# Kernel optimization log

Measured on AMD Instinct MI355X. Metric: run time of the kernel, lower is better.

## Reference

```python
import jax, jax.numpy as jnp
import numpy as np

B, C, D = 1024, 100, 768


def setup_inputs() -> dict:
    key = jax.random.key(0)
    k1, k2, k3, k4 = jax.random.split(key, 4)
    raw_features = jax.random.normal(k1, (B, D), dtype=jnp.float32)
    class_means = jax.random.normal(k2, (C, D), dtype=jnp.float32)
    # stand-in for per-class pinv of shrunk+normalized covariance
    class_inv_covs = jax.random.normal(k3, (C, D, D), dtype=jnp.float32) * 0.02
    # diag_std is positive (clamped at 1e-6 in the original)
    class_diags = jax.random.uniform(k4, (C, D), dtype=jnp.float32, minval=0.5, maxval=1.5)
    return {
        "raw_features": raw_features,
        "class_means": class_means,
        "class_inv_covs": class_inv_covs,
        "class_diags": class_diags,
    }


def reference(raw_features, class_means, class_inv_covs, class_diags):
    # Batched over classes: diff[b,c,d] = raw[b,d]/diag[c,d] - mean[c,d]/diag[c,d]
    diff = (raw_features[:, None, :] - class_means[None, :, :]) / class_diags[None, :, :]  # [B,C,D]
    # temp[b,c,e] = sum_d diff[b,c,d] * inv[c,d,e]  (the per-class diff @ inv_c)
    temp = jnp.einsum('bcd,cde->bce', diff, class_inv_covs)
    dist_sq = jnp.sum(temp * diff, axis=-1)  # [B,C]
    return -dist_sq  # scores_stack
```

## Files before the change

kernel.cpp:

```cpp
#include <hip/hip_runtime.h>
#include <hip/hip_bf16.h>

#define B_SZ 1024
#define C_SZ 100
#define D_SZ 768

#define BM 128
#define BN 256
#define BK 32
#define NKT (D_SZ / BK)
#define NTHREADS 512
#define TPC 24

#define A_HALF (BM * BK)
#define X_HALF (BN * BK)

#define TBL_ELEMS ((size_t)C_SZ * D_SZ)
#define AP_ELEMS  ((size_t)C_SZ * D_SZ * D_SZ)
#define RB_ELEMS  ((size_t)B_SZ * D_SZ)

typedef float f32x4 __attribute__((ext_vector_type(4)));
typedef short short8 __attribute__((ext_vector_type(8)));

__device__ __forceinline__ ushort f2bf(float f) {
    union { __hip_bfloat16 b; ushort u; } cv; cv.b = __float2bfloat16(f); return cv.u;
}
__device__ __forceinline__ float bf2f(ushort u) {
    union { __hip_bfloat16 b; ushort us; } cv; cv.us = u; return __bfloat162float(cv.b);
}
__device__ __forceinline__ void gload_lds16(const void* g, void* l) {
    __builtin_amdgcn_global_load_lds((const __attribute__((address_space(1))) void*)g,
                                     (__attribute__((address_space(3))) void*)l, 16, 0, 0);
}

__global__ __launch_bounds__(256) void prep_small(const float* __restrict__ mean,
                                                  const float* __restrict__ diag,
                                                  const float* __restrict__ raw,
                                                  float* __restrict__ rd,
                                                  float* __restrict__ md,
                                                  ushort* __restrict__ rb) {
    const int bx = (int)blockIdx.x;
    if (bx < 75) {
        const int i = (bx * 256 + (int)threadIdx.x) * 4;
        if (i < (int)TBL_ELEMS) {
            const f32x4 dv = *(const f32x4*)(diag + i);
            const f32x4 mv = *(const f32x4*)(mean + i);
            f32x4 r, m;
            r.x = 1.0f / dv.x; r.y = 1.0f / dv.y; r.z = 1.0f / dv.z; r.w = 1.0f / dv.w;
            m.x = mv.x * r.x;  m.y = mv.y * r.y;  m.z = mv.z * r.z;  m.w = mv.w * r.w;
            *(f32x4*)(rd + i) = r;
            *(f32x4*)(md + i) = m;
        }
    } else {
        const size_t i = (size_t)(bx - 75) * 256 + threadIdx.x;
        const f32x4 v0 = *(const f32x4*)(raw + i * 8);
        const f32x4 v1 = *(const f32x4*)(raw + i * 8 + 4);
        short8 p;
        p[0]=(short)f2bf(v0.x); p[1]=(short)f2bf(v0.y); p[2]=(short)f2bf(v0.z); p[3]=(short)f2bf(v0.w);
        p[4]=(short)f2bf(v1.x); p[5]=(short)f2bf(v1.y); p[6]=(short)f2bf(v1.z); p[7]=(short)f2bf(v1.w);
        *(short8*)(rb + i * 8) = p;
    }
}

__global__ __launch_bounds__(512) void conv_aprime(const float* __restrict__ inv,
                                                   const float* __restrict__ rd,
                                                   const float* __restrict__ md,
                                                   ushort* __restrict__ ap,
                                                   float* __restrict__ w) {
    const int lane = (int)threadIdx.x & 63;
    const int wv   = (int)threadIdx.x >> 6;
    const int ridx = (int)blockIdx.x * 8 + wv;
    const int c    = ridx / D_SZ;
    const float* arow = inv + (size_t)ridx * D_SZ;
    const float* rdc  = rd + (size_t)c * D_SZ;
    const float* mdc  = md + (size_t)c * D_SZ;
    ushort* aprow = ap + (size_t)ridx * D_SZ;
    float dot = 0.f;
    #pragma unroll
    for (int j = 0; j < 3; ++j) {
        const int e = j * 256 + lane * 4;
        const f32x4 a  = *(const f32x4*)(arow + e);
        const f32x4 r4 = *(const f32x4*)(rdc + e);
        const f32x4 m4 = *(const f32x4*)(mdc + e);
        dot += a.x * m4.x + a.y * m4.y + a.z * m4.z + a.w * m4.w;
        ushort4 p;
        p.x = f2bf(a.x * r4.x); p.y = f2bf(a.y * r4.y);
        p.z = f2bf(a.z * r4.z); p.w = f2bf(a.w * r4.w);
        *(ushort4*)(aprow + e) = p;
    }
    #pragma unroll
    for (int k = 1; k < 64; k <<= 1) dot += __shfl_xor(dot, k);
    if (lane == 0) w[ridx] = dot;
}

template <int MODE>
__global__ __launch_bounds__(NTHREADS, 4) void fecam_scores(
        const float* __restrict__ raw, const float* __restrict__ mean,
        const float* __restrict__ diag, const float* __restrict__ inv,
        const float* __restrict__ rdT, const float* __restrict__ mdT,
        const float* __restrict__ wT,
        const ushort* __restrict__ apAll, const ushort* __restrict__ rbAll,
        float* __restrict__ out) {
    __shared__ __align__(16) ushort aLds[2 * A_HALF];
    __shared__ __align__(16) ushort xLds[2 * X_HALF];
    __shared__ float red[8 * 64];

    const int tid = (int)threadIdx.x;
    const int bx  = (int)blockIdx.x;

    const int x = bx & 7;
    const int slot0 = bx >> 3;
    const int nCls  = (x < 4) ? 13 : 12;
    const int baseC = (x < 4) ? x * 13 : 52 + (x - 4) * 12;
    const int ci = slot0 / TPC;
    if (ci >= nCls) return;
    const int t  = slot0 % TPC;
    const int c  = baseC + ci;
    const int d0 = (t >> 2) * BM;
    const int b0 = (t & 3) * BN;

    const int lane = tid & 63;
    const int wid  = tid >> 6;
    const int wm   = wid >> 2;
    const int wn   = wid & 3;
    const int l15  = lane & 15;
    const int l4   = lane >> 4;

    const ushort* apc = apAll + (size_t)c * D_SZ * D_SZ;
    const float*  Af  = inv + (size_t)c * D_SZ * D_SZ;

    auto stage_a = [&](ushort* dst, int kt) {
        const int s = tid;
        const int r = s >> 2;
        const int q = (s & 3) ^ ((r >> 1) & 3);
        if constexpr (MODE == 2) {
            gload_lds16(apc + (size_t)(d0 + r) * D_SZ + kt * BK + q * 8, dst + s * 8);
        } else {
            const float* gp = Af + (size_t)(d0 + r) * D_SZ + kt * BK + q * 8;
            const f32x4 a0 = *(const f32x4*)gp;
            const f32x4 a1 = *(const f32x4*)(gp + 4);
            short8 p;
            p[0]=(short)f2bf(a0.x); p[1]=(short)f2bf(a0.y); p[2]=(short)f2bf(a0.z); p[3]=(short)f2bf(a0.w);
            p[4]=(short)f2bf(a1.x); p[5]=(short)f2bf(a1.y); p[6]=(short)f2bf(a1.z); p[7]=(short)f2bf(a1.w);
            *(short8*)(dst + s * 8) = p;
        }
    };
    auto stage_x = [&](ushort* dst, int kt) {
        #pragma unroll
        for (int i = 0; i < 2; ++i) {
            const int s = tid + i * NTHREADS;
            const int r = s >> 2;
            const int q = (s & 3) ^ ((r >> 1) & 3);
            const int e = kt * BK + q * 8;
            if constexpr (MODE == 2) {
                gload_lds16(rbAll + (size_t)(b0 + r) * D_SZ + e, dst + s * 8);
            } else {
                const float* rp = raw + (size_t)(b0 + r) * D_SZ + e;
                const f32x4 r0 = *(const f32x4*)rp, r1 = *(const f32x4*)(rp + 4);
                const f32x4 mm0 = *(const f32x4*)(mean + (size_t)c * D_SZ + e);
                const f32x4 mm1 = *(const f32x4*)(mean + (size_t)c * D_SZ + e + 4);
                const f32x4 gg0 = *(const f32x4*)(diag + (size_t)c * D_SZ + e);
                const f32x4 gg1 = *(const f32x4*)(diag + (size_t)c * D_SZ + e + 4);
                short8 p;
                p[0]=(short)f2bf((r0.x-mm0.x)/gg0.x); p[1]=(short)f2bf((r0.y-mm0.y)/gg0.y);
                p[2]=(short)f2bf((r0.z-mm0.z)/gg0.z); p[3]=(short)f2bf((r0.w-mm0.w)/gg0.w);
                p[4]=(short)f2bf((r1.x-mm1.x)/gg1.x); p[5]=(short)f2bf((r1.y-mm1.y)/gg1.y);
                p[6]=(short)f2bf((r1.z-mm1.z)/gg1.z); p[7]=(short)f2bf((r1.w-mm1.w)/gg1.w);
                *(short8*)(dst + s * 8) = p;
            }
        }
    };

    stage_a(aLds, 0);
    stage_x(xLds, 0);
    __syncthreads();

    f32x4 acc[4][4] = {};

    const int fch = l4 ^ ((l15 >> 1) & 3);
    for (int kt = 0; kt < NKT; ++kt) {
        const int cur = kt & 1;
        if (kt + 1 < NKT) {
            stage_a(aLds + (cur ^ 1) * A_HALF, kt + 1);
            stage_x(xLds + (cur ^ 1) * X_HALF, kt + 1);
        }
        const ushort* ab = aLds + cur * A_HALF;
        const ushort* xb = xLds + cur * X_HALF;
        short8 xf[4];
        #pragma unroll
        for (int n = 0; n < 4; ++n)
            xf[n] = *(const short8*)(xb + ((wn * 64 + n * 16 + l15) * 4 + fch) * 8);
        #pragma unroll
        for (int m = 0; m < 4; ++m) {
            const short8 af = *(const short8*)(ab + ((wm * 64 + m * 16 + l15) * 4 + fch) * 8);
            #pragma unroll
            for (int n = 0; n < 4; ++n)
                acc[m][n] = __builtin_amdgcn_mfma_f32_16x16x32_bf16(af, xf[n], acc[m][n], 0, 0, 0);
        }
        __syncthreads();
    }

    float v[4] = {};
    #pragma unroll
    for (int m = 0; m < 4; ++m) {
        const int dd = d0 + wm * 64 + m * 16 + l4 * 4;
        f32x4 rd4, md4, w4;
        if constexpr (MODE == 2) {
            rd4 = *(const f32x4*)(rdT + (size_t)c * D_SZ + dd);
            md4 = *(const f32x4*)(mdT + (size_t)c * D_SZ + dd);
            w4  = *(const f32x4*)(wT + (size_t)c * D_SZ + dd);
        } else {
            const f32x4 mm4 = *(const f32x4*)(mean + (size_t)c * D_SZ + dd);
            const f32x4 gg4 = *(const f32x4*)(diag + (size_t)c * D_SZ + dd);
            rd4.x = 1.0f/gg4.x; rd4.y = 1.0f/gg4.y; rd4.z = 1.0f/gg4.z; rd4.w = 1.0f/gg4.w;
            md4.x = mm4.x*rd4.x; md4.y = mm4.y*rd4.y; md4.z = mm4.z*rd4.z; md4.w = mm4.w*rd4.w;
            w4.x = 0.f; w4.y = 0.f; w4.z = 0.f; w4.w = 0.f;
        }
        #pragma unroll
        for (int n = 0; n < 4; ++n) {
            const int bl = b0 + wn * 64 + n * 16 + l15;
            const f32x4 rv = *(const f32x4*)(raw + (size_t)bl * D_SZ + dd);
            v[n] += (w4.x - acc[m][n][0]) * (rv.x * rd4.x - md4.x)
                  + (w4.y - acc[m][n][1]) * (rv.y * rd4.y - md4.y)
                  + (w4.z - acc[m][n][2]) * (rv.z * rd4.z - md4.z)
                  + (w4.w - acc[m][n][3]) * (rv.w * rd4.w - md4.w);
        }
    }
    #pragma unroll
    for (int n = 0; n < 4; ++n) {
        v[n] += __shfl_xor(v[n], 16);
        v[n] += __shfl_xor(v[n], 32);
    }
    if (lane < 16) {
        #pragma unroll
        for (int n = 0; n < 4; ++n) red[wid * 64 + n * 16 + l15] = v[n];
    }
    __syncthreads();
    if (tid < BN) {
        const int wno = tid >> 6;
        const int off = tid & 63;
        const float p = red[wno * 64 + off] + red[(4 + wno) * 64 + off];
        atomicAdd(out + (size_t)(b0 + tid) * C_SZ + c, p);
    }
}

extern "C" void kernel_launch(void* const* d_in, const int* in_sizes, int n_in,
                              void* d_out, int out_size, void* d_ws, size_t ws_size,
                              hipStream_t stream) {
    const float* raw  = (const float*)d_in[0];
    const float* mean = (const float*)d_in[1];
    const float* inv  = (const float*)d_in[2];
    const float* diag = (const float*)d_in[3];
    float* out = (float*)d_out;

    const size_t TBL_B = TBL_ELEMS * 4;
    const size_t AP_B  = AP_ELEMS * 2;
    const size_t RB_B  = RB_ELEMS * 2;
    const size_t need  = 3 * TBL_B + AP_B + RB_B;

    hipMemsetAsync(d_out, 0, (size_t)out_size * sizeof(float), stream);
    dim3 grid(8 * 13 * TPC);

    if (ws_size >= need) {
        float*  rdT = (float*)d_ws;
        float*  mdT = (float*)((char*)d_ws + TBL_B);
        float*  wT  = (float*)((char*)d_ws + 2 * TBL_B);
        ushort* ap  = (ushort*)((char*)d_ws + 3 * TBL_B);
        ushort* rb  = (ushort*)((char*)d_ws + 3 * TBL_B + AP_B);
        prep_small<<<75 + 384, 256, 0, stream>>>(mean, diag, raw, rdT, mdT, rb);
        conv_aprime<<<9600, 512, 0, stream>>>(inv, rdT, mdT, ap, wT);
        fecam_scores<2><<<grid, NTHREADS, 0, stream>>>(raw, mean, diag, inv,
                                                       rdT, mdT, wT, ap, rb, out);
    } else {
        fecam_scores<0><<<grid, NTHREADS, 0, stream>>>(raw, mean, diag, inv,
                                                       nullptr, nullptr, nullptr,
                                                       nullptr, nullptr, out);
    }
}
```

Before: 238.8 us.

## Enlarge GEMM tile to 256x256x64 with interleaved async LDS prefetch

The main scores kernel moves from 128x256x32 tiles to 256x256x64 tiles, doubling each warp's M fragments to 8x4 accumulators and halving the block count per class. The next K-tile is prefetched with global_load_lds in four parts interleaved with the MFMA phases, using explicit barriers, s_setprio around the MFMA blocks and an 8-way XOR swizzle. The old fp32 path becomes a separate fallback kernel. The larger tile cuts redundant A/X traffic per FLOP and raises MFMA density, at the cost of more registers and lower occupancy (launch bounds 2).

```diff
diff --git a/kernel.cpp b/kernel.cpp
--- a/kernel.cpp
+++ b/kernel.cpp
@@ -5,15 +5,14 @@
 #define C_SZ 100
 #define D_SZ 768
 
-#define BM 128
+#define BM 256
 #define BN 256
-#define BK 32
+#define BK 64
 #define NKT (D_SZ / BK)
 #define NTHREADS 512
-#define TPC 24
-
-#define A_HALF (BM * BK)
-#define X_HALF (BN * BK)
+#define TPC 12
+#define A_TILE (BM * BK)
+#define X_TILE (BN * BK)
 
 #define TBL_ELEMS ((size_t)C_SZ * D_SZ)
 #define AP_ELEMS  ((size_t)C_SZ * D_SZ * D_SZ)
@@ -93,17 +92,14 @@
     if (lane == 0) w[ridx] = dot;
 }
 
-template <int MODE>
-__global__ __launch_bounds__(NTHREADS, 4) void fecam_scores(
-        const float* __restrict__ raw, const float* __restrict__ mean,
-        const float* __restrict__ diag, const float* __restrict__ inv,
+__global__ __launch_bounds__(NTHREADS, 2) void fecam_scores8(
+        const float* __restrict__ raw,
         const float* __restrict__ rdT, const float* __restrict__ mdT,
         const float* __restrict__ wT,
         const ushort* __restrict__ apAll, const ushort* __restrict__ rbAll,
         float* __restrict__ out) {
-    __shared__ __align__(16) ushort aLds[2 * A_HALF];
-    __shared__ __align__(16) ushort xLds[2 * X_HALF];
-    __shared__ float red[8 * 64];
+    __shared__ __align__(16) ushort aLds[2 * A_TILE];
+    __shared__ __align__(16) ushort xLds[2 * X_TILE];
 
     const int tid = (int)threadIdx.x;
     const int bx  = (int)blockIdx.x;
@@ -126,96 +122,74 @@
     const int l15  = lane & 15;
     const int l4   = lane >> 4;
 
-    const ushort* apc = apAll + (size_t)c * D_SZ * D_SZ;
-    const float*  Af  = inv + (size_t)c * D_SZ * D_SZ;
-
-    auto stage_a = [&](ushort* dst, int kt) {
-        const int s = tid;
-        const int r = s >> 2;
-        const int q = (s & 3) ^ ((r >> 1) & 3);
-        if constexpr (MODE == 2) {
-            gload_lds16(apc + (size_t)(d0 + r) * D_SZ + kt * BK + q * 8, dst + s * 8);
-        } else {
-            const float* gp = Af + (size_t)(d0 + r) * D_SZ + kt * BK + q * 8;
-            const f32x4 a0 = *(const f32x4*)gp;
-            const f32x4 a1 = *(const f32x4*)(gp + 4);
-            short8 p;
-            p[0]=(short)f2bf(a0.x); p[1]=(short)f2bf(a0.y); p[2]=(short)f2bf(a0.z); p[3]=(short)f2bf(a0.w);
-            p[4]=(short)f2bf(a1.x); p[5]=(short)f2bf(a1.y); p[6]=(short)f2bf(a1.z); p[7]=(short)f2bf(a1.w);
-            *(short8*)(dst + s * 8) = p;
-        }
+    const ushort* apc = apAll + (size_t)c * D_SZ * D_SZ + (size_t)d0 * D_SZ;
+    const ushort* rbc = rbAll + (size_t)b0 * D_SZ;
+
+    auto stage_part = [&](ushort* dstbase, const ushort* src, int kt, int i) {
+        const int s = tid + i * NTHREADS;
+        const int r = s >> 3;
+        const int q = (s & 7) ^ (r & 7);
+        gload_lds16(src + (size_t)r * D_SZ + kt * BK + q * 8, dstbase + s * 8);
     };
-    auto stage_x = [&](ushort* dst, int kt) {
-        #pragma unroll
-        for (int i = 0; i < 2; ++i) {
-            const int s = tid + i * NTHREADS;
-            const int r = s >> 2;
-            const int q = (s & 3) ^ ((r >> 1) & 3);
-            const int e = kt * BK + q * 8;
-            if constexpr (MODE == 2) {
-                gload_lds16(rbAll + (size_t)(b0 + r) * D_SZ + e, dst + s * 8);
-            } else {
-                const float* rp = raw + (size_t)(b0 + r) * D_SZ + e;
-                const f32x4 r0 = *(const f32x4*)rp, r1 = *(const f32x4*)(rp + 4);
-                const f32x4 mm0 = *(const f32x4*)(mean + (size_t)c * D_SZ + e);
-                const f32x4 mm1 = *(const f32x4*)(mean + (size_t)c * D_SZ + e + 4);
-                const f32x4 gg0 = *(const f32x4*)(diag + (size_t)c * D_SZ + e);
-                const f32x4 gg1 = *(const f32x4*)(diag + (size_t)c * D_SZ + e + 4);
-                short8 p;
-                p[0]=(short)f2bf((r0.x-mm0.x)/gg0.x); p[1]=(short)f2bf((r0.y-mm0.y)/gg0.y);
-                p[2]=(short)f2bf((r0.z-mm0.z)/gg0.z); p[3]=(short)f2bf((r0.w-mm0.w)/gg0.w);
-                p[4]=(short)f2bf((r1.x-mm1.x)/gg1.x); p[5]=(short)f2bf((r1.y-mm1.y)/gg1.y);
-                p[6]=(short)f2bf((r1.z-mm1.z)/gg1.z); p[7]=(short)f2bf((r1.w-mm1.w)/gg1.w);
-                *(short8*)(dst + s * 8) = p;
+
+    #pragma unroll
+    for (int i = 0; i < 4; ++i) {
+        stage_part(aLds, apc, 0, i);
+        stage_part(xLds, rbc, 0, i);
+    }
+    asm volatile("s_waitcnt vmcnt(0)" ::: "memory");
+    __builtin_amdgcn_s_barrier();
+
+    f32x4 acc[8][4] = {};
+    const int swz = l15 & 7;
+
+    for (int kt = 0; kt < NKT; ++kt) {
+        const int bf = kt & 1;
+        const ushort* ab = aLds + bf * A_TILE;
+        const ushort* xb = xLds + bf * X_TILE;
+        ushort* anx = aLds + (bf ^ 1) * A_TILE;
+        ushort* xnx = xLds + (bf ^ 1) * X_TILE;
+        const bool pre = (kt + 1 < NKT);
+        short8 xf[4];
+        #pragma unroll
+        for (int p = 0; p < 4; ++p) {
+            const int kk = p >> 1;
+            const int mh = p & 1;
+            const int ch = (kk * 4 + l4) ^ swz;
+            if (mh == 0) {
+                #pragma unroll
+                for (int n = 0; n < 4; ++n)
+                    xf[n] = *(const short8*)(xb + ((wn * 64 + n * 16 + l15) * 8 + ch) * 8);
             }
-        }
-    };
-
-    stage_a(aLds, 0);
-    stage_x(xLds, 0);
-    __syncthreads();
-
-    f32x4 acc[4][4] = {};
-
-    const int fch = l4 ^ ((l15 >> 1) & 3);
-    for (int kt = 0; kt < NKT; ++kt) {
-        const int cur = kt & 1;
-        if (kt + 1 < NKT) {
-            stage_a(aLds + (cur ^ 1) * A_HALF, kt + 1);
-            stage_x(xLds + (cur ^ 1) * X_HALF, kt + 1);
-        }
-        const ushort* ab = aLds + cur * A_HALF;
-        const ushort* xb = xLds + cur * X_HALF;
-        short8 xf[4];
-        #pragma unroll
-        for (int n = 0; n < 4; ++n)
-            xf[n] = *(const short8*)(xb + ((wn * 64 + n * 16 + l15) * 4 + fch) * 8);
-        #pragma unroll
-        for (int m = 0; m < 4; ++m) {
-            const short8 af = *(const short8*)(ab + ((wm * 64 + m * 16 + l15) * 4 + fch) * 8);
+            short8 af[4];
             #pragma unroll
-            for (int n = 0; n < 4; ++n)
-                acc[m][n] = __builtin_amdgcn_mfma_f32_16x16x32_bf16(af, xf[n], acc[m][n], 0, 0, 0);
-        }
-        __syncthreads();
+            for (int m2 = 0; m2 < 4; ++m2)
+                af[m2] = *(const short8*)(ab + ((wm * 128 + (mh * 4 + m2) * 16 + l15) * 8 + ch) * 8);
+            if (pre) {
+                stage_part(anx, apc, kt + 1, p);
+                stage_part(xnx, rbc, kt + 1, p);
+            }
+            __builtin_amdgcn_s_barrier();
+            __builtin_amdgcn_s_setprio(1);
+            #pragma unroll
+            for (int m2 = 0; m2 < 4; ++m2)
+                #pragma unroll
+                for (int n = 0; n < 4; ++n)
+                    acc[mh * 4 + m2][n] = __builtin_amdgcn_mfma_f32_16x16x32_bf16(
+                        af[m2], xf[n], acc[mh * 4 + m2][n], 0, 0, 0);
+            __builtin_amdgcn_s_setprio(0);
+            if (p == 3 && pre) asm volatile("s_waitcnt vmcnt(0)" ::: "memory");
+            __builtin_amdgcn_s_barrier();
+        }
     }
 
     float v[4] = {};
     #pragma unroll
-    for (int m = 0; m < 4; ++m) {
-        const int dd = d0 + wm * 64 + m * 16 + l4 * 4;
-        f32x4 rd4, md4, w4;
-        if constexpr (MODE == 2) {
-            rd4 = *(const f32x4*)(rdT + (size_t)c * D_SZ + dd);
-            md4 = *(const f32x4*)(mdT + (size_t)c * D_SZ + dd);
-            w4  = *(const f32x4*)(wT + (size_t)c * D_SZ + dd);
-        } else {
-            const f32x4 mm4 = *(const f32x4*)(mean + (size_t)c * D_SZ + dd);
-            const f32x4 gg4 = *(const f32x4*)(diag + (size_t)c * D_SZ + dd);
-            rd4.x = 1.0f/gg4.x; rd4.y = 1.0f/gg4.y; rd4.z = 1.0f/gg4.z; rd4.w = 1.0f/gg4.w;
-            md4.x = mm4.x*rd4.x; md4.y = mm4.y*rd4.y; md4.z = mm4.z*rd4.z; md4.w = mm4.w*rd4.w;
-            w4.x = 0.f; w4.y = 0.f; w4.z = 0.f; w4.w = 0.f;
-        }
+    for (int m = 0; m < 8; ++m) {
+        const int dd = d0 + wm * 128 + m * 16 + l4 * 4;
+        const f32x4 rd4 = *(const f32x4*)(rdT + (size_t)c * D_SZ + dd);
+        const f32x4 md4 = *(const f32x4*)(mdT + (size_t)c * D_SZ + dd);
+        const f32x4 w4  = *(const f32x4*)(wT + (size_t)c * D_SZ + dd);
         #pragma unroll
         for (int n = 0; n < 4; ++n) {
             const int bl = b0 + wn * 64 + n * 16 + l15;
@@ -231,12 +205,139 @@
         v[n] += __shfl_xor(v[n], 16);
         v[n] += __shfl_xor(v[n], 32);
     }
+    float* red = (float*)aLds;
     if (lane < 16) {
         #pragma unroll
         for (int n = 0; n < 4; ++n) red[wid * 64 + n * 16 + l15] = v[n];
     }
     __syncthreads();
     if (tid < BN) {
+        const int wno = tid >> 6;
+        const int off = tid & 63;
+        const float p = red[wno * 64 + off] + red[(4 + wno) * 64 + off];
+        atomicAdd(out + (size_t)(b0 + tid) * C_SZ + c, p);
+    }
+}
+
+__global__ __launch_bounds__(512, 4) void fecam_fallback(
+        const float* __restrict__ raw, const float* __restrict__ mean,
+        const float* __restrict__ diag, const float* __restrict__ inv,
+        float* __restrict__ out) {
+    __shared__ __align__(16) ushort aLds[2 * 128 * 32];
+    __shared__ __align__(16) ushort xLds[2 * 256 * 32];
+    __shared__ float red[8 * 64];
+
+    const int tid = (int)threadIdx.x;
+    const int bx  = (int)blockIdx.x;
+    const int x = bx & 7;
+    const int slot0 = bx >> 3;
+    const int nCls  = (x < 4) ? 13 : 12;
+    const int baseC = (x < 4) ? x * 13 : 52 + (x - 4) * 12;
+    const int ci = slot0 / 24;
+    if (ci >= nCls) return;
+    const int t  = slot0 % 24;
+    const int c  = baseC + ci;
+    const int d0 = (t >> 2) * 128;
+    const int b0 = (t & 3) * 256;
+
+    const int lane = tid & 63;
+    const int wid  = tid >> 6;
+    const int wm   = wid >> 2;
+    const int wn   = wid & 3;
+    const int l15  = lane & 15;
+    const int l4   = lane >> 4;
+    const float* Af = inv + (size_t)c * D_SZ * D_SZ;
+
+    auto stage_a = [&](ushort* dst, int kt) {
+        const int s = tid;
+        const int r = s >> 2;
+        const int q = (s & 3) ^ ((r >> 1) & 3);
+        const float* gp = Af + (size_t)(d0 + r) * D_SZ + kt * 32 + q * 8;
+        const f32x4 a0 = *(const f32x4*)gp;
+        const f32x4 a1 = *(const f32x4*)(gp + 4);
+        short8 p;
+        p[0]=(short)f2bf(a0.x); p[1]=(short)f2bf(a0.y); p[2]=(short)f2bf(a0.z); p[3]=(short)f2bf(a0.w);
+        p[4]=(short)f2bf(a1.x); p[5]=(short)f2bf(a1.y); p[6]=(short)f2bf(a1.z); p[7]=(short)f2bf(a1.w);
+        *(short8*)(dst + s * 8) = p;
+    };
+    auto stage_x = [&](ushort* dst, int kt) {
+        #pragma unroll
+        for (int i = 0; i < 2; ++i) {
+            const int s = tid + i * 512;
+            const int r = s >> 2;
+            const int q = (s & 3) ^ ((r >> 1) & 3);
+            const int e = kt * 32 + q * 8;
+            const float* rp = raw + (size_t)(b0 + r) * D_SZ + e;
+            const f32x4 r0 = *(const f32x4*)rp, r1 = *(const f32x4*)(rp + 4);
+            const f32x4 mm0 = *(const f32x4*)(mean + (size_t)c * D_SZ + e);
+            const f32x4 mm1 = *(const f32x4*)(mean + (size_t)c * D_SZ + e + 4);
+            const f32x4 gg0 = *(const f32x4*)(diag + (size_t)c * D_SZ + e);
+            const f32x4 gg1 = *(const f32x4*)(diag + (size_t)c * D_SZ + e + 4);
+            short8 p;
+            p[0]=(short)f2bf((r0.x-mm0.x)/gg0.x); p[1]=(short)f2bf((r0.y-mm0.y)/gg0.y);
+            p[2]=(short)f2bf((r0.z-mm0.z)/gg0.z); p[3]=(short)f2bf((r0.w-mm0.w)/gg0.w);
+            p[4]=(short)f2bf((r1.x-mm1.x)/gg1.x); p[5]=(short)f2bf((r1.y-mm1.y)/gg1.y);
+            p[6]=(short)f2bf((r1.z-mm1.z)/gg1.z); p[7]=(short)f2bf((r1.w-mm1.w)/gg1.w);
+            *(short8*)(dst + s * 8) = p;
+        }
+    };
+
+    stage_a(aLds, 0);
+    stage_x(xLds, 0);
+    __syncthreads();
+    f32x4 acc[4][4] = {};
+    const int fch = l4 ^ ((l15 >> 1) & 3);
+    for (int kt = 0; kt < 24; ++kt) {
+        const int cur = kt & 1;
+        if (kt + 1 < 24) {
+            stage_a(aLds + (cur ^ 1) * 128 * 32, kt + 1);
+            stage_x(xLds + (cur ^ 1) * 256 * 32, kt + 1);
+        }
+        const ushort* ab = aLds + cur * 128 * 32;
+        const ushort* xb = xLds + cur * 256 * 32;
+        short8 xf[4];
+        #pragma unroll
+        for (int n = 0; n < 4; ++n)
+            xf[n] = *(const short8*)(xb + ((wn * 64 + n * 16 + l15) * 4 + fch) * 8);
+        #pragma unroll
+        for (int m = 0; m < 4; ++m) {
+            const short8 af = *(const short8*)(ab + ((wm * 64 + m * 16 + l15) * 4 + fch) * 8);
+            #pragma unroll
+            for (int n = 0; n < 4; ++n)
+                acc[m][n] = __builtin_amdgcn_mfma_f32_16x16x32_bf16(af, xf[n], acc[m][n], 0, 0, 0);
+        }
+        __syncthreads();
+    }
+    float v[4] = {};
+    #pragma unroll
+    for (int m = 0; m < 4; ++m) {
+        const int dd = d0 + wm * 64 + m * 16 + l4 * 4;
+        const f32x4 mm4 = *(const f32x4*)(mean + (size_t)c * D_SZ + dd);
+        const f32x4 gg4 = *(const f32x4*)(diag + (size_t)c * D_SZ + dd);
+        f32x4 rd4, md4;
+        rd4.x = 1.0f/gg4.x; rd4.y = 1.0f/gg4.y; rd4.z = 1.0f/gg4.z; rd4.w = 1.0f/gg4.w;
+        md4.x = mm4.x*rd4.x; md4.y = mm4.y*rd4.y; md4.z = mm4.z*rd4.z; md4.w = mm4.w*rd4.w;
+        #pragma unroll
+        for (int n = 0; n < 4; ++n) {
+            const int bl = b0 + wn * 64 + n * 16 + l15;
+            const f32x4 rv = *(const f32x4*)(raw + (size_t)bl * D_SZ + dd);
+            v[n] += (0.f - acc[m][n][0]) * (rv.x * rd4.x - md4.x)
+                  + (0.f - acc[m][n][1]) * (rv.y * rd4.y - md4.y)
+                  + (0.f - acc[m][n][2]) * (rv.z * rd4.z - md4.z)
+                  + (0.f - acc[m][n][3]) * (rv.w * rd4.w - md4.w);
+        }
+    }
+    #pragma unroll
+    for (int n = 0; n < 4; ++n) {
+        v[n] += __shfl_xor(v[n], 16);
+        v[n] += __shfl_xor(v[n], 32);
+    }
+    if (lane < 16) {
+        #pragma unroll
+        for (int n = 0; n < 4; ++n) red[wid * 64 + n * 16 + l15] = v[n];
+    }
+    __syncthreads();
+    if (tid < 256) {
         const int wno = tid >> 6;
         const int off = tid & 63;
         const float p = red[wno * 64 + off] + red[(4 + wno) * 64 + off];
@@ -259,7 +360,6 @@
     const size_t need  = 3 * TBL_B + AP_B + RB_B;
 
     hipMemsetAsync(d_out, 0, (size_t)out_size * sizeof(float), stream);
-    dim3 grid(8 * 13 * TPC);
 
     if (ws_size >= need) {
         float*  rdT = (float*)d_ws;
@@ -269,11 +369,10 @@
         ushort* rb  = (ushort*)((char*)d_ws + 3 * TBL_B + AP_B);
         prep_small<<<75 + 384, 256, 0, stream>>>(mean, diag, raw, rdT, mdT, rb);
         conv_aprime<<<9600, 512, 0, stream>>>(inv, rdT, mdT, ap, wT);
-        fecam_scores<2><<<grid, NTHREADS, 0, stream>>>(raw, mean, diag, inv,
-                                                       rdT, mdT, wT, ap, rb, out);
+        dim3 grid(8 * 13 * TPC);
+        fecam_scores8<<<grid, NTHREADS, 0, stream>>>(raw, rdT, mdT, wT, ap, rb, out);
     } else {
-        fecam_scores<0><<<grid, NTHREADS, 0, stream>>>(raw, mean, diag, inv,
-                                                       nullptr, nullptr, nullptr,
-                                                       nullptr, nullptr, out);
-    }
-}
+        dim3 grid(8 * 13 * 24);
+        fecam_fallback<<<grid, 512, 0, stream>>>(raw, mean, diag, inv, out);
+    }
+}
```

New measurement: 238.7 us. No clear change (-0.0%).

## Triple-buffer LDS staging with a single barrier and explicit vmcnt waits

Applied to the files above, without the earlier changes.

Replaces the double-buffered LDS pipeline with three slots that prefetch two k-tiles ahead. Each iteration now has one barrier, placed before the stage, and in the direct global-to-LDS mode it waits on vmcnt(3) instead of draining all outstanding loads. This is meant to hide more global load latency and remove one sync per k-step. In exchange it needs 50% more LDS, which may reduce occupancy from the requested 4 blocks per CU, and it relies on the hand-written vmcnt count matching the number of loads issued per stage.

```diff
diff --git a/kernel.cpp b/kernel.cpp
--- a/kernel.cpp
+++ b/kernel.cpp
@@ -11,9 +11,10 @@
 #define NKT (D_SZ / BK)
 #define NTHREADS 512
 #define TPC 24
-
-#define A_HALF (BM * BK)
-#define X_HALF (BN * BK)
+#define NSLOT 3
+
+#define A_BUF (BM * BK)
+#define X_BUF (BN * BK)
 
 #define TBL_ELEMS ((size_t)C_SZ * D_SZ)
 #define AP_ELEMS  ((size_t)C_SZ * D_SZ * D_SZ)
@@ -101,8 +102,8 @@
         const float* __restrict__ wT,
         const ushort* __restrict__ apAll, const ushort* __restrict__ rbAll,
         float* __restrict__ out) {
-    __shared__ __align__(16) ushort aLds[2 * A_HALF];
-    __shared__ __align__(16) ushort xLds[2 * X_HALF];
+    __shared__ __align__(16) ushort aLds[NSLOT * A_BUF];
+    __shared__ __align__(16) ushort xLds[NSLOT * X_BUF];
     __shared__ float red[8 * 64];
 
     const int tid = (int)threadIdx.x;
@@ -129,23 +130,24 @@
     const ushort* apc = apAll + (size_t)c * D_SZ * D_SZ;
     const float*  Af  = inv + (size_t)c * D_SZ * D_SZ;
 
-    auto stage_a = [&](ushort* dst, int kt) {
-        const int s = tid;
-        const int r = s >> 2;
-        const int q = (s & 3) ^ ((r >> 1) & 3);
-        if constexpr (MODE == 2) {
-            gload_lds16(apc + (size_t)(d0 + r) * D_SZ + kt * BK + q * 8, dst + s * 8);
-        } else {
-            const float* gp = Af + (size_t)(d0 + r) * D_SZ + kt * BK + q * 8;
-            const f32x4 a0 = *(const f32x4*)gp;
-            const f32x4 a1 = *(const f32x4*)(gp + 4);
-            short8 p;
-            p[0]=(short)f2bf(a0.x); p[1]=(short)f2bf(a0.y); p[2]=(short)f2bf(a0.z); p[3]=(short)f2bf(a0.w);
-            p[4]=(short)f2bf(a1.x); p[5]=(short)f2bf(a1.y); p[6]=(short)f2bf(a1.z); p[7]=(short)f2bf(a1.w);
-            *(short8*)(dst + s * 8) = p;
-        }
-    };
-    auto stage_x = [&](ushort* dst, int kt) {
+    auto stage = [&](int sl, int kt) {
+        {
+            const int s = tid;
+            const int r = s >> 2;
+            const int q = (s & 3) ^ ((r >> 1) & 3);
+            if constexpr (MODE == 2) {
+                gload_lds16(apc + (size_t)(d0 + r) * D_SZ + kt * BK + q * 8,
+                            aLds + sl * A_BUF + s * 8);
+            } else {
+                const float* gp = Af + (size_t)(d0 + r) * D_SZ + kt * BK + q * 8;
+                const f32x4 a0 = *(const f32x4*)gp;
+                const f32x4 a1 = *(const f32x4*)(gp + 4);
+                short8 p;
+                p[0]=(short)f2bf(a0.x); p[1]=(short)f2bf(a0.y); p[2]=(short)f2bf(a0.z); p[3]=(short)f2bf(a0.w);
+                p[4]=(short)f2bf(a1.x); p[5]=(short)f2bf(a1.y); p[6]=(short)f2bf(a1.z); p[7]=(short)f2bf(a1.w);
+                *(short8*)(aLds + sl * A_BUF + s * 8) = p;
+            }
+        }
         #pragma unroll
         for (int i = 0; i < 2; ++i) {
             const int s = tid + i * NTHREADS;
@@ -153,7 +155,8 @@
             const int q = (s & 3) ^ ((r >> 1) & 3);
             const int e = kt * BK + q * 8;
             if constexpr (MODE == 2) {
-                gload_lds16(rbAll + (size_t)(b0 + r) * D_SZ + e, dst + s * 8);
+                gload_lds16(rbAll + (size_t)(b0 + r) * D_SZ + e,
+                            xLds + sl * X_BUF + s * 8);
             } else {
                 const float* rp = raw + (size_t)(b0 + r) * D_SZ + e;
                 const f32x4 r0 = *(const f32x4*)rp, r1 = *(const f32x4*)(rp + 4);
@@ -166,26 +169,29 @@
                 p[2]=(short)f2bf((r0.z-mm0.z)/gg0.z); p[3]=(short)f2bf((r0.w-mm0.w)/gg0.w);
                 p[4]=(short)f2bf((r1.x-mm1.x)/gg1.x); p[5]=(short)f2bf((r1.y-mm1.y)/gg1.y);
                 p[6]=(short)f2bf((r1.z-mm1.z)/gg1.z); p[7]=(short)f2bf((r1.w-mm1.w)/gg1.w);
-                *(short8*)(dst + s * 8) = p;
+                *(short8*)(xLds + sl * X_BUF + s * 8) = p;
             }
         }
     };
 
-    stage_a(aLds, 0);
-    stage_x(xLds, 0);
-    __syncthreads();
+    stage(0, 0);
+    stage(1, 1);
 
     f32x4 acc[4][4] = {};
 
     const int fch = l4 ^ ((l15 >> 1) & 3);
     for (int kt = 0; kt < NKT; ++kt) {
-        const int cur = kt & 1;
-        if (kt + 1 < NKT) {
-            stage_a(aLds + (cur ^ 1) * A_HALF, kt + 1);
-            stage_x(xLds + (cur ^ 1) * X_HALF, kt + 1);
-        }
-        const ushort* ab = aLds + cur * A_HALF;
-        const ushort* xb = xLds + cur * X_HALF;
+        const int cs = kt % 3;
+        if constexpr (MODE == 2) {
+            if (kt < NKT - 1) asm volatile("s_waitcnt vmcnt(3)" ::: "memory");
+            else              asm volatile("s_waitcnt vmcnt(0)" ::: "memory");
+            __builtin_amdgcn_s_barrier();
+        } else {
+            __syncthreads();
+        }
+        if (kt + 2 < NKT) stage((kt + 2) % 3, kt + 2);
+        const ushort* ab = aLds + cs * A_BUF;
+        const ushort* xb = xLds + cs * X_BUF;
         short8 xf[4];
         #pragma unroll
         for (int n = 0; n < 4; ++n)
@@ -197,7 +203,6 @@
             for (int n = 0; n < 4; ++n)
                 acc[m][n] = __builtin_amdgcn_mfma_f32_16x16x32_bf16(af, xf[n], acc[m][n], 0, 0, 0);
         }
-        __syncthreads();
     }
 
     float v[4] = {};
@@ -231,6 +236,7 @@
         v[n] += __shfl_xor(v[n], 16);
         v[n] += __shfl_xor(v[n], 32);
     }
+    __syncthreads();
     if (lane < 16) {
         #pragma unroll
         for (int n = 0; n < 4; ++n) red[wid * 64 + n * 16 + l15] = v[n];
```

New measurement: 248.6 us. 4.1% more time.
